# Optimization experiments

Measured on AMD Instinct MI355X. Metric: run time of the kernel, lower is better.

The kernel has to match this reference:

```python
import jax, jax.numpy as jnp
import numpy as np

N, D, H = 2048, 128, 40


def setup_inputs() -> dict:
    key = jax.random.key(0)
    kx, kw, kv = jax.random.split(key, 3)
    X = jax.random.normal(kx, (N, D), dtype=jnp.float32)
    # nn.Parameter(torch.randn(D, D) / D) per head, stacked over H
    W = jax.random.normal(kw, (H, D, D), dtype=jnp.float32) / D
    V = jax.random.normal(kv, (H, D, D), dtype=jnp.float32) / D
    return {"X": X, "W": W, "V": V}


def reference(X, W, V):
    d = X.shape[1]
    # scores[h] = X @ W[h] @ X.T / sqrt(D)   -> [H, N, N]
    XW = jnp.einsum("nd,hde->hne", X, W)
    scores = jnp.einsum("hne,me->hnm", XW, X) / jnp.sqrt(jnp.asarray(d, X.dtype))
    # softmax over dim=1 of the 2D per-head score matrix == last axis here
    weights = jax.nn.softmax(scores, axis=-1) + 1e-8
    # A[h] = weights[h] @ X @ V[h]; output = sum over heads -> [N, D]
    XV = jnp.einsum("md,hde->hme", X, V)
    out = jnp.einsum("hnm,hme->ne", weights, XV)
    return out
```

## Files before the change

### kernel.cpp

```cpp
#include <hip/hip_runtime.h>
#include <hip/hip_bf16.h>
#include <stdint.h>

#define N 2048
#define D 128
#define H 40
#define NT 16

typedef __attribute__((ext_vector_type(8))) short short8;
typedef __attribute__((ext_vector_type(4))) float float4v;
typedef __attribute__((ext_vector_type(16))) float float16v;
typedef __attribute__((ext_vector_type(4))) _Float16 half4v;

static __device__ __forceinline__ unsigned short f32_to_bf16(float f) {
  unsigned int u = __builtin_bit_cast(unsigned int, f);
  unsigned int rounding = 0x7FFFu + ((u >> 16) & 1u);
  return (unsigned short)((u + rounding) >> 16);
}

static __device__ __forceinline__ unsigned int pk2(float lo, float hi) {
  return (unsigned int)f32_to_bf16(lo) | ((unsigned int)f32_to_bf16(hi) << 16);
}

static __device__ __forceinline__ unsigned int pk2f(float lo, float hi) {
  unsigned int a = __builtin_bit_cast(unsigned int, lo) + 0x8000u;
  unsigned int b = __builtin_bit_cast(unsigned int, hi) + 0x8000u;
  return __builtin_amdgcn_perm(b, a, 0x07060302u);
}

static __device__ __forceinline__ unsigned long long pack4(float x0, float x1,
                                                           float x2, float x3) {
  return (unsigned long long)pk2(x0, x1) | ((unsigned long long)pk2(x2, x3) << 32);
}

static __device__ __forceinline__ float fast_exp2(float x) {
#if __has_builtin(__builtin_amdgcn_exp2f)
  return __builtin_amdgcn_exp2f(x);
#else
  return __expf(0.69314718056f * x);
#endif
}

static __device__ __forceinline__ float bf2f(unsigned short u) {
  unsigned int x = ((unsigned int)u) << 16;
  return __builtin_bit_cast(float, x);
}

static __device__ __forceinline__ long long mk64(unsigned int lo, unsigned int hi) {
  return (long long)(((unsigned long long)hi << 32) | lo);
}

static __device__ __forceinline__ void load_lds16(const void* g, void* l) {
  __builtin_amdgcn_global_load_lds(
      (const __attribute__((address_space(1))) unsigned int*)g,
      (__attribute__((address_space(3))) unsigned int*)l, 16, 0, 0);
}

#define MFMA32(a, b, c) __builtin_amdgcn_mfma_f32_32x32x16_bf16((a), (b), (c), 0, 0, 0)
#define MFMA8(a, b, c) __builtin_amdgcn_mfma_f32_32x32x16_fp8_fp8((a), (b), (c), 0, 0, 0)

static __device__ __forceinline__ void regs_to_bfrags(const float16v c, int hh,
                                                      short8& f0, short8& f1) {
  unsigned int a0 = pk2f(c[0], c[1]),   a1 = pk2f(c[2], c[3]);
  unsigned int a2 = pk2f(c[4], c[5]),   a3 = pk2f(c[6], c[7]);
  unsigned int a4 = pk2f(c[8], c[9]),   a5 = pk2f(c[10], c[11]);
  unsigned int a6 = pk2f(c[12], c[13]), a7 = pk2f(c[14], c[15]);
  unsigned int x0 = __shfl_xor(hh ? a0 : a2, 32);
  unsigned int x1 = __shfl_xor(hh ? a1 : a3, 32);
  unsigned int x2 = __shfl_xor(hh ? a4 : a6, 32);
  unsigned int x3 = __shfl_xor(hh ? a5 : a7, 32);
  uint4 u0 = {hh ? x0 : a0, hh ? x1 : a1, hh ? a2 : x0, hh ? a3 : x1};
  uint4 u1 = {hh ? x2 : a4, hh ? x3 : a5, hh ? a6 : x2, hh ? a7 : x3};
  f0 = __builtin_bit_cast(short8, u0);
  f1 = __builtin_bit_cast(short8, u1);
}

static __device__ __forceinline__ void regs_to_f8frags(const float16v c, int hh,
                                                       long long& f0, long long& f1) {
  const float s = 64.0f;
  int v0 = __builtin_amdgcn_cvt_pk_fp8_f32(c[0] * s, c[1] * s, 0, false);
  v0 = __builtin_amdgcn_cvt_pk_fp8_f32(c[2] * s, c[3] * s, v0, true);
  int v1 = __builtin_amdgcn_cvt_pk_fp8_f32(c[4] * s, c[5] * s, 0, false);
  v1 = __builtin_amdgcn_cvt_pk_fp8_f32(c[6] * s, c[7] * s, v1, true);
  int v2 = __builtin_amdgcn_cvt_pk_fp8_f32(c[8] * s, c[9] * s, 0, false);
  v2 = __builtin_amdgcn_cvt_pk_fp8_f32(c[10] * s, c[11] * s, v2, true);
  int v3 = __builtin_amdgcn_cvt_pk_fp8_f32(c[12] * s, c[13] * s, 0, false);
  v3 = __builtin_amdgcn_cvt_pk_fp8_f32(c[14] * s, c[15] * s, v3, true);
  int t0 = __shfl_xor(hh ? v0 : v1, 32);
  int t1 = __shfl_xor(hh ? v2 : v3, 32);
  f0 = hh ? mk64((unsigned)t0, (unsigned)v1) : mk64((unsigned)v0, (unsigned)t0);
  f1 = hh ? mk64((unsigned)t1, (unsigned)v3) : mk64((unsigned)v2, (unsigned)t1);
}

static __device__ __forceinline__ void regs_to_pfrags(const float16v s, int hh,
                                                      float& lsum, short8& f0,
                                                      short8& f1) {
  float e[16];
  float acc = 0.0f;
#pragma unroll
  for (int i = 0; i < 16; i++) { e[i] = fast_exp2(s[i] * 0.015625f); acc += e[i]; }
  lsum += acc;
  unsigned int a0 = pk2f(e[0], e[1]),   a1 = pk2f(e[2], e[3]);
  unsigned int a2 = pk2f(e[4], e[5]),   a3 = pk2f(e[6], e[7]);
  unsigned int a4 = pk2f(e[8], e[9]),   a5 = pk2f(e[10], e[11]);
  unsigned int a6 = pk2f(e[12], e[13]), a7 = pk2f(e[14], e[15]);
  unsigned int x0 = __shfl_xor(hh ? a0 : a2, 32);
  unsigned int x1 = __shfl_xor(hh ? a1 : a3, 32);
  unsigned int x2 = __shfl_xor(hh ? a4 : a6, 32);
  unsigned int x3 = __shfl_xor(hh ? a5 : a7, 32);
  uint4 u0 = {hh ? x0 : a0, hh ? x1 : a1, hh ? a2 : x0, hh ? a3 : x1};
  uint4 u1 = {hh ? x2 : a4, hh ? x3 : a5, hh ? a6 : x2, hh ? a7 : x3};
  f0 = __builtin_bit_cast(short8, u0);
  f1 = __builtin_bit_cast(short8, u1);
}

static __device__ __forceinline__ void stage_64x256(const char* gbase, size_t stride,
                                                    char* lds, int wave, int lane) {
#pragma unroll
  for (int i = 0; i < 4; i++) {
    int r = wave * 16 + i * 4 + (lane >> 4);
    int us = (lane & 15) ^ (r & 15);
    load_lds16(gbase + (size_t)r * stride + us * 16, lds + (wave * 16 + i * 4) * 256);
  }
}
static __device__ __forceinline__ void stage_128x256(const char* gbase, size_t stride,
                                                     char* lds, int wave, int lane) {
#pragma unroll
  for (int i = 0; i < 8; i++) {
    int r = wave * 32 + i * 4 + (lane >> 4);
    int us = (lane & 15) ^ (r & 15);
    load_lds16(gbase + (size_t)r * stride + us * 16, lds + (wave * 32 + i * 4) * 256);
  }
}
static __device__ __forceinline__ void stage_128x128(const char* gbase, size_t stride,
                                                     int colOff, char* lds, int wave,
                                                     int lane) {
#pragma unroll
  for (int i = 0; i < 4; i++) {
    int m = wave * 16 + i * 4 + (lane >> 4);
    int u = (lane & 15) ^ (m & 15);
    int grow = 2 * m + (u >> 3);
    load_lds16(gbase + (size_t)grow * stride + colOff + (u & 7) * 16,
               lds + (wave * 16 + i * 4) * 256);
  }
}
static __device__ __forceinline__ void stage_k8(const char* gbase, char* lds,
                                                int wave, int lane) {
#pragma unroll
  for (int i = 0; i < 2; i++) {
    int m = wave * 8 + i * 4 + (lane >> 4);
    int u = (lane & 15) ^ (m & 15);
    int grow = 2 * m + (u >> 3);
    load_lds16(gbase + (size_t)grow * 128 + (u & 7) * 16,
               lds + (wave * 8 + i * 4) * 256);
  }
}
static __device__ __forceinline__ short8 read_macro(const char* lds, int row, int kunit) {
  int m = row >> 1;
  int u = ((row & 1) << 3) | kunit;
  return *(const short8*)(lds + m * 256 + ((u ^ (m & 15)) * 16));
}

__global__ __launch_bounds__(256)
void prep_kernel(const float* __restrict__ X, const float* __restrict__ W,
                 const float* __restrict__ V, unsigned short* __restrict__ Xb,
                 unsigned short* __restrict__ XbT, unsigned char* __restrict__ Xf8,
                 unsigned short* __restrict__ Wt, unsigned short* __restrict__ Vt) {
  const int tid = threadIdx.x;
  __shared__ __align__(16) unsigned short Lt[128 * 136];
  if (blockIdx.x < 16) {
    const int n0 = blockIdx.x * 128;
    for (int i = tid; i < 128 * 32; i += 256) {
      int row = i >> 5, c4 = (i & 31) * 4;
      float4v x = *(const float4v*)(X + (size_t)(n0 + row) * D + c4);
      unsigned long long p = pack4(x.x, x.y, x.z, x.w);
      *(unsigned long long*)(Lt + row * 136 + c4) = p;
      *(unsigned long long*)(Xb + (size_t)(n0 + row) * D + c4) = p;
    }
    __syncthreads();
    for (int i = tid; i < 128 * 16; i += 256) {
      int d = i >> 4, g = i & 15;
      short8 v;
#pragma unroll
      for (int j = 0; j < 8; j++) v[j] = (short)Lt[(g * 8 + j) * 136 + d];
      *(short8*)(XbT + (size_t)d * N + n0 + g * 8) = v;
    }
    for (int i = tid; i < 128 * 8; i += 256) {
      int row = i >> 3, c = i & 7, t = c >> 1, o8 = (c & 1) * 8;
      const unsigned short* lp = Lt + row * 136;
      int d0 = t * 32 + o8, d1 = t * 32 + 16 + o8;
      short8 xa = *(const short8*)(lp + d0);
      short8 xb = *(const short8*)(lp + d1);
      int w0 = __builtin_amdgcn_cvt_pk_fp8_f32(bf2f(xa[0]), bf2f(xa[1]), 0, false);
      w0 = __builtin_amdgcn_cvt_pk_fp8_f32(bf2f(xa[2]), bf2f(xa[3]), w0, true);
      int w1 = __builtin_amdgcn_cvt_pk_fp8_f32(bf2f(xa[4]), bf2f(xa[5]), 0, false);
      w1 = __builtin_amdgcn_cvt_pk_fp8_f32(bf2f(xa[6]), bf2f(xa[7]), w1, true);
      int w2 = __builtin_amdgcn_cvt_pk_fp8_f32(bf2f(xb[0]), bf2f(xb[1]), 0, false);
      w2 = __builtin_amdgcn_cvt_pk_fp8_f32(bf2f(xb[2]), bf2f(xb[3]), w2, true);
      int w3 = __builtin_amdgcn_cvt_pk_fp8_f32(bf2f(xb[4]), bf2f(xb[5]), 0, false);
      w3 = __builtin_amdgcn_cvt_pk_fp8_f32(bf2f(xb[6]), bf2f(xb[7]), w3, true);
      uint4 st = {(unsigned)w0, (unsigned)w1, (unsigned)w2, (unsigned)w3};
      *(uint4*)(Xf8 + (size_t)(n0 + row) * 128 + c * 16) = st;
    }
  } else {
    const int b = blockIdx.x - 16;
    const int mat = (b >= H) ? 1 : 0;
    const int h = mat ? b - H : b;
    const float* src = (mat ? V : W) + (size_t)h * D * D;
    unsigned short* dst = (mat ? Vt : Wt) + (size_t)h * D * D;
    const float scale = mat ? 1.0f : 0.1275174313f;
    for (int i = tid; i < 128 * 32; i += 256) {
      int d = i >> 5, e4 = (i & 31) * 4;
      float4v w = *(const float4v*)(src + d * D + e4);
      Lt[(e4 + 0) * 136 + d] = f32_to_bf16(w.x * scale);
      Lt[(e4 + 1) * 136 + d] = f32_to_bf16(w.y * scale);
      Lt[(e4 + 2) * 136 + d] = f32_to_bf16(w.z * scale);
      Lt[(e4 + 3) * 136 + d] = f32_to_bf16(w.w * scale);
    }
    __syncthreads();
    for (int i = tid; i < 128 * 16; i += 256) {
      int e = i >> 4, u = i & 15;
      *(uint4*)((char*)dst + (size_t)e * 256 + u * 16) =
          *(const uint4*)((const char*)Lt + (size_t)e * 272 + u * 16);
    }
  }
}

__global__ __launch_bounds__(256)
void qprep_kernel(const unsigned short* __restrict__ Xb,
                  const unsigned short* __restrict__ Wt,
                  unsigned char* __restrict__ Qf8g) {
  __shared__ __align__(16) char smem[32768];
  const int bx = blockIdx.x;
  const int h = bx >> 4;
  const int q0 = (bx & 15) << 7;
  const int tid = threadIdx.x;
  const int wave = tid >> 6, lane = tid & 63;
  const int l = lane & 31, hh = lane >> 5;

  stage_128x256((const char*)(Wt + (size_t)h * D * D), 256, smem, wave, lane);
  short8 xfr[8];
#pragma unroll
  for (int dk = 0; dk < 8; dk++)
    xfr[dk] = *(const short8*)((const char*)Xb +
              (size_t)(q0 + wave * 32 + l) * 256 + dk * 32 + hh * 16);
  __syncthreads();

  float16v qa[4];
#pragma unroll
  for (int et = 0; et < 4; et++) qa[et] = (float16v)0.0f;
#pragma unroll
  for (int et = 0; et < 4; et++) {
    const int r = et * 32 + l;
#pragma unroll
    for (int dk = 0; dk < 8; dk++) {
      short8 wa = *(const short8*)(smem + r * 256 + (((2 * dk + hh) ^ (r & 15)) * 16));
      qa[et] = MFMA32(wa, xfr[dk], qa[et]);
    }
  }
  char* base = (char*)Qf8g + ((size_t)bx * 4 + wave) * 4096;
#pragma unroll
  for (int et = 0; et < 4; et++) {
    long long f0, f1;
    regs_to_f8frags(qa[et], hh, f0, f1);
    uint4 st = {(unsigned)(unsigned long long)f0,
                (unsigned)((unsigned long long)f0 >> 32),
                (unsigned)(unsigned long long)f1,
                (unsigned)((unsigned long long)f1 >> 32)};
    *(uint4*)(base + et * 1024 + lane * 16) = st;
  }
}

__global__ __launch_bounds__(256)
void attn_kernel(const unsigned char* __restrict__ Qf8g,
                 const unsigned char* __restrict__ Xf8,
                 const unsigned short* __restrict__ XbT,
                 const unsigned short* __restrict__ Vt,
                 unsigned short* __restrict__ Opart, float* __restrict__ Lsum) {
  __shared__ __align__(16) char smem[49152];
  char* XA = smem;
  char* XB = smem + 16384;
  char* KA = smem + 32768;
  char* KB = smem + 40960;
  const int bx = blockIdx.x;
  const int kh = bx & 1;
  const int qt = (bx >> 1) & 15;
  const int q0 = qt << 7;
  const int h = bx >> 5;
  const int tid = threadIdx.x;
  const int wave = tid >> 6, lane = tid & 63;
  const int l = lane & 31, hh = lane >> 5;

  const char* Xf8B = (const char*)Xf8;
  const char* XbTB = (const char*)XbT;
  const char* VtB = (const char*)(Vt + (size_t)h * D * D);
  const int kbase = kh * (N / 2);

  stage_k8(Xf8B + (size_t)kbase * 128, KA, wave, lane);
  stage_128x128(XbTB, 4096, kbase * 2, XA, wave, lane);
  long long qf8[8];
  {
    const char* qp = (const char*)Qf8g + (((size_t)h * 16 + qt) * 4 + wave) * 4096;
#pragma unroll
    for (int i = 0; i < 4; i++) {
      uint4 v = *(const uint4*)(qp + i * 1024 + lane * 16);
      qf8[2 * i] = mk64(v.x, v.y);
      qf8[2 * i + 1] = mk64(v.z, v.w);
    }
  }
  float16v Tacc[4];
#pragma unroll
  for (int dt = 0; dt < 4; dt++) Tacc[dt] = (float16v)0.0f;
  float lsum = 0.0f;
  __syncthreads();

  for (int kt = 0; kt < NT; kt++) {
    const char* curK = (kt & 1) ? KB : KA;
    const char* curX = (kt & 1) ? XB : XA;
    char* altK = (kt & 1) ? KA : KB;
    char* altX = (kt & 1) ? XA : XB;
    if (kt + 1 < NT) {
      const int k0n = kbase + (kt + 1) * 64;
      stage_k8(Xf8B + (size_t)k0n * 128, altK, wave, lane);
      stage_128x128(XbTB, 4096, k0n * 2, altX, wave, lane);
    } else {
      stage_64x256(VtB, 256, altX, wave, lane);
    }
    float16v s0 = (float16v)0.0f, s1 = (float16v)0.0f;
    {
      const int m0 = l >> 1, r0 = (l & 1) << 3;
      const int m1 = (32 + l) >> 1, r1 = (l & 1) << 3;
#pragma unroll
      for (int t = 0; t < 4; t++) {
        int u0 = (r0 | (t * 2 + hh)) ^ (m0 & 15);
        int u1 = (r1 | (t * 2 + hh)) ^ (m1 & 15);
        uint4 w0 = *(const uint4*)(curK + m0 * 256 + u0 * 16);
        uint4 w1 = *(const uint4*)(curK + m1 * 256 + u1 * 16);
        s0 = MFMA8(mk64(w0.x, w0.y), qf8[2 * t], s0);
        s1 = MFMA8(mk64(w1.x, w1.y), qf8[2 * t], s1);
        s0 = MFMA8(mk64(w0.z, w0.w), qf8[2 * t + 1], s0);
        s1 = MFMA8(mk64(w1.z, w1.w), qf8[2 * t + 1], s1);
      }
    }
    short8 pf0[2], pf1[2];
    regs_to_pfrags(s0, hh, lsum, pf0[0], pf0[1]);
    regs_to_pfrags(s1, hh, lsum, pf1[0], pf1[1]);
#pragma unroll
    for (int kk = 0; kk < 2; kk++)
#pragma unroll
      for (int dt = 0; dt < 4; dt++) {
        short8 xt0 = read_macro(curX, dt * 32 + l, kk * 2 + hh);
        Tacc[dt] = MFMA32(xt0, pf0[kk], Tacc[dt]);
        short8 xt1 = read_macro(curX, dt * 32 + l, 4 + kk * 2 + hh);
        Tacc[dt] = MFMA32(xt1, pf1[kk], Tacc[dt]);
      }
    __syncthreads();
  }

  float tot = lsum + __shfl_xor(lsum, 32);
  if (hh == 0) Lsum[(size_t)(h * 2 + kh) * N + q0 + wave * 32 + l] = tot;

  stage_64x256(VtB + 64 * 256, 256, XB, wave, lane);
  short8 tb[8];
#pragma unroll
  for (int dt = 0; dt < 4; dt++)
    regs_to_bfrags(Tacc[dt], hh, tb[2 * dt], tb[2 * dt + 1]);

  float16v oacc[4];
#pragma unroll
  for (int et = 0; et < 4; et++) oacc[et] = (float16v)0.0f;
#pragma unroll
  for (int et = 0; et < 2; et++) {
    const int r = et * 32 + l;
#pragma unroll
    for (int dk = 0; dk < 8; dk++) {
      short8 va = *(const short8*)(XA + r * 256 + (((2 * dk + hh) ^ (r & 15)) * 16));
      oacc[et] = MFMA32(va, tb[dk], oacc[et]);
    }
  }
  __syncthreads();
#pragma unroll
  for (int et = 2; et < 4; et++) {
    const int r = (et - 2) * 32 + l;
#pragma unroll
    for (int dk = 0; dk < 8; dk++) {
      short8 va = *(const short8*)(XB + r * 256 + (((2 * dk + hh) ^ (r & 15)) * 16));
      oacc[et] = MFMA32(va, tb[dk], oacc[et]);
    }
  }

  unsigned short* Oph = Opart + (size_t)(h * 2 + kh) * N * D;
#pragma unroll
  for (int pass = 0; pass < 2; pass++) {
    __syncthreads();
    const int qrow = wave * 32 + l;
#pragma unroll
    for (int etL = 0; etL < 2; etL++) {
      int et = pass * 2 + etL;
#pragma unroll
      for (int g = 0; g < 4; g++) {
        int unit = etL * 8 + 2 * g + hh;
        float4v v;
        v.x = oacc[et][4 * g + 0];
        v.y = oacc[et][4 * g + 1];
        v.z = oacc[et][4 * g + 2];
        v.w = oacc[et][4 * g + 3];
        *(float4v*)(smem + qrow * 256 + ((unit ^ (qrow & 15)) * 16)) = v;
      }
    }
    __syncthreads();
#pragma unroll
    for (int i = 0; i < 8; i++) {
      int idx = i * 256 + tid;
      int qr = idx >> 4, up = idx & 15, u = up ^ (qr & 15);
      float4v v = *(const float4v*)(smem + qr * 256 + up * 16);
      auto h0 = __builtin_amdgcn_cvt_pkrtz(v.x, v.y);
      auto h1 = __builtin_amdgcn_cvt_pkrtz(v.z, v.w);
      uint2 st = {__builtin_bit_cast(unsigned int, h0),
                  __builtin_bit_cast(unsigned int, h1)};
      *(uint2*)(Oph + (size_t)(q0 + qr) * D + pass * 64 + u * 4) = st;
    }
  }
}

__global__ __launch_bounds__(256)
void reduce_kernel(const unsigned short* __restrict__ Opart,
                   const float* __restrict__ Lsum, float* __restrict__ out) {
  int idx = blockIdx.x * 256 + threadIdx.x;
  int n = idx >> 5;
  const uint2* base = (const uint2*)Opart;
  float4v acc = (float4v)0.0f;
#pragma unroll 8
  for (int h = 0; h < H; h++) {
    float lt = Lsum[(size_t)(2 * h) * N + n] + Lsum[(size_t)(2 * h + 1) * N + n];
    float il = __builtin_amdgcn_rcpf(lt);
    uint2 a = base[(size_t)(2 * h) * (N * D / 4) + idx];
    uint2 b = base[(size_t)(2 * h + 1) * (N * D / 4) + idx];
    float4v fa = __builtin_convertvector(__builtin_bit_cast(half4v, a), float4v);
    float4v fb = __builtin_convertvector(__builtin_bit_cast(half4v, b), float4v);
    acc += (fa + fb) * il;
  }
  *(float4v*)(out + (size_t)idx * 4) = acc;
}

extern "C" void kernel_launch(void* const* d_in, const int* in_sizes, int n_in,
                              void* d_out, int out_size, void* d_ws, size_t ws_size,
                              hipStream_t stream) {
  const float* X = (const float*)d_in[0];
  const float* W = (const float*)d_in[1];
  const float* V = (const float*)d_in[2];
  float* out = (float*)d_out;

  unsigned short* Xb = (unsigned short*)d_ws;
  unsigned short* XbT = Xb + (size_t)N * D;
  unsigned short* Wt = XbT + (size_t)N * D;
  unsigned short* Vt = Wt + (size_t)H * D * D;
  unsigned char* Xf8 = (unsigned char*)(Vt + (size_t)H * D * D);
  unsigned char* Qf8g = Xf8 + (size_t)N * D;
  unsigned short* Opart = (unsigned short*)(Qf8g + (size_t)H * 16 * 4 * 4096);
  float* Lsum = (float*)(Opart + (size_t)H * 2 * N * D);

  prep_kernel<<<dim3(16 + 2 * H), 256, 0, stream>>>(X, W, V, Xb, XbT, Xf8, Wt, Vt);
  qprep_kernel<<<dim3(16 * H), 256, 0, stream>>>(Xb, Wt, Qf8g);
  attn_kernel<<<dim3(NT * 2 * H), 256, 0, stream>>>(Qf8g, Xf8, XbT, Vt, Opart, Lsum);
  reduce_kernel<<<dim3(N * D / 4 / 256), 256, 0, stream>>>(Opart, Lsum, out);
}
```

Before: 196.2 us.

## Single-buffer X tile to cut LDS to 32KB for higher occupancy

Replaces the double-buffered X tile (two 16KB buffers) with a single 16KB buffer that is loaded in the same iteration it is used. An extra barrier separates the load from the MFMA reads. LDS per block drops from 48KB to 32KB so more blocks can be resident per CU. V staging now reuses the K buffer and the X buffer. The cost is that the X load is no longer prefetched one iteration ahead, which exposes its latency and adds a barrier per iteration.

```diff
diff --git a/kernel.cpp b/kernel.cpp
--- a/kernel.cpp
+++ b/kernel.cpp
@@ -277,11 +277,10 @@
                  const unsigned short* __restrict__ XbT,
                  const unsigned short* __restrict__ Vt,
                  unsigned short* __restrict__ Opart, float* __restrict__ Lsum) {
-  __shared__ __align__(16) char smem[49152];
-  char* XA = smem;
-  char* XB = smem + 16384;
-  char* KA = smem + 32768;
-  char* KB = smem + 40960;
+  __shared__ __align__(16) char smem[32768];
+  char* Xbuf = smem;
+  char* KA = smem + 16384;
+  char* KB = smem + 24576;
   const int bx = blockIdx.x;
   const int kh = bx & 1;
   const int qt = (bx >> 1) & 15;
@@ -297,7 +296,6 @@
   const int kbase = kh * (N / 2);
 
   stage_k8(Xf8B + (size_t)kbase * 128, KA, wave, lane);
-  stage_128x128(XbTB, 4096, kbase * 2, XA, wave, lane);
   long long qf8[8];
   {
     const char* qp = (const char*)Qf8g + (((size_t)h * 16 + qt) * 4 + wave) * 4096;
@@ -316,24 +314,19 @@
 
   for (int kt = 0; kt < NT; kt++) {
     const char* curK = (kt & 1) ? KB : KA;
-    const char* curX = (kt & 1) ? XB : XA;
     char* altK = (kt & 1) ? KA : KB;
-    char* altX = (kt & 1) ? XA : XB;
-    if (kt + 1 < NT) {
-      const int k0n = kbase + (kt + 1) * 64;
-      stage_k8(Xf8B + (size_t)k0n * 128, altK, wave, lane);
-      stage_128x128(XbTB, 4096, k0n * 2, altX, wave, lane);
-    } else {
-      stage_64x256(VtB, 256, altX, wave, lane);
-    }
+    const int k0 = kbase + kt * 64;
+    stage_128x128(XbTB, 4096, k0 * 2, Xbuf, wave, lane);
+    if (kt + 1 < NT)
+      stage_k8(Xf8B + (size_t)(k0 + 64) * 128, altK, wave, lane);
     float16v s0 = (float16v)0.0f, s1 = (float16v)0.0f;
     {
       const int m0 = l >> 1, r0 = (l & 1) << 3;
-      const int m1 = (32 + l) >> 1, r1 = (l & 1) << 3;
+      const int m1 = (32 + l) >> 1;
 #pragma unroll
       for (int t = 0; t < 4; t++) {
         int u0 = (r0 | (t * 2 + hh)) ^ (m0 & 15);
-        int u1 = (r1 | (t * 2 + hh)) ^ (m1 & 15);
+        int u1 = (r0 | (t * 2 + hh)) ^ (m1 & 15);
         uint4 w0 = *(const uint4*)(curK + m0 * 256 + u0 * 16);
         uint4 w1 = *(const uint4*)(curK + m1 * 256 + u1 * 16);
         s0 = MFMA8(mk64(w0.x, w0.y), qf8[2 * t], s0);
@@ -345,13 +338,14 @@
     short8 pf0[2], pf1[2];
     regs_to_pfrags(s0, hh, lsum, pf0[0], pf0[1]);
     regs_to_pfrags(s1, hh, lsum, pf1[0], pf1[1]);
+    __syncthreads();
 #pragma unroll
     for (int kk = 0; kk < 2; kk++)
 #pragma unroll
       for (int dt = 0; dt < 4; dt++) {
-        short8 xt0 = read_macro(curX, dt * 32 + l, kk * 2 + hh);
+        short8 xt0 = read_macro(Xbuf, dt * 32 + l, kk * 2 + hh);
         Tacc[dt] = MFMA32(xt0, pf0[kk], Tacc[dt]);
-        short8 xt1 = read_macro(curX, dt * 32 + l, 4 + kk * 2 + hh);
+        short8 xt1 = read_macro(Xbuf, dt * 32 + l, 4 + kk * 2 + hh);
         Tacc[dt] = MFMA32(xt1, pf1[kk], Tacc[dt]);
       }
     __syncthreads();
@@ -360,11 +354,13 @@
   float tot = lsum + __shfl_xor(lsum, 32);
   if (hh == 0) Lsum[(size_t)(h * 2 + kh) * N + q0 + wave * 32 + l] = tot;
 
-  stage_64x256(VtB + 64 * 256, 256, XB, wave, lane);
+  stage_64x256(VtB, 256, KA, wave, lane);
+  stage_64x256(VtB + 64 * 256, 256, Xbuf, wave, lane);
   short8 tb[8];
 #pragma unroll
   for (int dt = 0; dt < 4; dt++)
     regs_to_bfrags(Tacc[dt], hh, tb[2 * dt], tb[2 * dt + 1]);
+  __syncthreads();
 
   float16v oacc[4];
 #pragma unroll
@@ -374,17 +370,16 @@
     const int r = et * 32 + l;
 #pragma unroll
     for (int dk = 0; dk < 8; dk++) {
-      short8 va = *(const short8*)(XA + r * 256 + (((2 * dk + hh) ^ (r & 15)) * 16));
+      short8 va = *(const short8*)(KA + r * 256 + (((2 * dk + hh) ^ (r & 15)) * 16));
       oacc[et] = MFMA32(va, tb[dk], oacc[et]);
     }
   }
-  __syncthreads();
 #pragma unroll
   for (int et = 2; et < 4; et++) {
     const int r = (et - 2) * 32 + l;
 #pragma unroll
     for (int dk = 0; dk < 8; dk++) {
-      short8 va = *(const short8*)(XB + r * 256 + (((2 * dk + hh) ^ (r & 15)) * 16));
+      short8 va = *(const short8*)(Xbuf + r * 256 + (((2 * dk + hh) ^ (r & 15)) * 16));
       oacc[et] = MFMA32(va, tb[dk], oacc[et]);
     }
   }
```

Measured after the change: 195.6 us. No clear change (-0.3%).
